# Kernel tuning notes

Measured on AMD Instinct MI355X. Metric: run time of the kernel, lower is better.

Reference implementation:

```python
import jax, jax.numpy as jnp
import numpy as np

C_Z = 128
H = 4
D = C_Z // H          # head_dim = 32
BASE = 2 * D // 2     # base_feature_dim = feature_map_multiplier*head_dim//2 = 32
BSZ, S = 1, 256
EPS_LN = 1e-5


def _lin_params(key, fan_in, fan_out):
    kw, kb = jax.random.split(key)
    bound = 1.0 / np.sqrt(fan_in)
    w = jax.random.uniform(kw, (fan_out, fan_in), jnp.float32, -bound, bound)
    b = jax.random.uniform(kb, (fan_out,), jnp.float32, -bound, bound)
    return w, b


def setup_inputs() -> dict:
    key = jax.random.key(0)
    ks = jax.random.split(key, 9)
    z = jax.random.normal(ks[0], (BSZ, S, S, C_Z), jnp.float32)
    pair_mask = jax.random.randint(ks[1], (BSZ, S, S), 0, 2, jnp.int32)
    q_w, q_b = _lin_params(ks[2], C_Z, C_Z)
    k_w, k_b = _lin_params(ks[3], C_Z, C_Z)
    v_w, v_b = _lin_params(ks[4], C_Z, C_Z)
    qf_w, qf_b = _lin_params(ks[5], D, BASE)
    kf_w, kf_b = _lin_params(ks[6], D, BASE)
    g_w, g_b = _lin_params(ks[7], C_Z, C_Z)
    o_w, o_b = _lin_params(ks[8], C_Z, C_Z)
    return {
        'z': z, 'pair_mask': pair_mask,
        'ln_w': jnp.ones((C_Z,), jnp.float32), 'ln_b': jnp.zeros((C_Z,), jnp.float32),
        'q_w': q_w, 'q_b': q_b, 'k_w': k_w, 'k_b': k_b, 'v_w': v_w, 'v_b': v_b,
        'qf_w': qf_w, 'qf_b': qf_b, 'kf_w': kf_w, 'kf_b': kf_b,
        'g_w': g_w, 'g_b': g_b, 'o_w': o_w, 'o_b': o_b,
    }


def _feature_map(t, w, b):
    m = jnp.clip(t @ w.T + b, -8.0, 8.0)
    return jnp.concatenate([jnp.exp(m), jnp.exp(-m)], axis=-1)


def reference(z, pair_mask, ln_w, ln_b, q_w, q_b, k_w, k_b, v_w, v_b,
              qf_w, qf_b, kf_w, kf_b, g_w, g_b, o_w, o_b):
    bsz, seq, _, c = z.shape
    h, d = H, c // H
    mask = pair_mask.astype(z.dtype)                         # [B,S,S]

    # LayerNorm over last dim
    mu = jnp.mean(z, axis=-1, keepdims=True)
    var = jnp.mean(jnp.square(z - mu), axis=-1, keepdims=True)
    zn = (z - mu) * jax.lax.rsqrt(var + EPS_LN) * ln_w + ln_b

    z_rows = zn.reshape(bsz * seq, seq, c)                   # [BS, N, C]
    row_mask = mask.reshape(bsz * seq, seq)[:, None, :, None]  # [BS,1,N,1]

    def proj(w, b):
        return (z_rows @ w.T + b).reshape(bsz * seq, seq, h, d).transpose(0, 2, 1, 3)

    q = proj(q_w, q_b)                                       # [BS,H,N,D]
    k = proj(k_w, k_b)
    v = proj(v_w, v_b) * row_mask

    qf = _feature_map(q, qf_w, qf_b)                         # [BS,H,N,F]
    kf = _feature_map(k, kf_w, kf_b) * row_mask

    kv = jnp.einsum('bhnd,bhne->bhde', kf, v)                # [BS,H,F,D]
    k_sum = kf.sum(axis=-2)                                  # [BS,H,F]
    denom = jnp.maximum(jnp.einsum('bhnd,bhd->bhn', qf, k_sum), 1e-6)
    out = jnp.einsum('bhnd,bhde->bhne', qf, kv) / denom[..., None]

    out = out.transpose(0, 2, 1, 3).reshape(bsz * seq, seq, c)
    gate = jax.nn.sigmoid(z_rows @ g_w.T + g_b)
    out = (gate * out) @ o_w.T + o_b
    out = out.reshape(bsz, seq, seq, c)
    return out * mask[..., None]
```

## Files before the change

### kernel.cpp

```cpp
#include <hip/hip_runtime.h>
#include <stdint.h>

#define DEV __device__ __forceinline__

typedef unsigned short u16;
typedef unsigned int u32;
typedef short bh8 __attribute__((ext_vector_type(8)));
typedef float f32x4 __attribute__((ext_vector_type(4)));

DEV float bf2f(u16 v){ return __uint_as_float(((u32)v)<<16); }
DEV u16 f2bf(float f){
    u32 x = __float_as_uint(f);
    x += 0x7fffu + ((x>>16)&1u);
    return (u16)(x>>16);
}
DEV void cvt8(int4 r, float* f){
    u32 a=(u32)r.x, b=(u32)r.y, c=(u32)r.z, d=(u32)r.w;
    f[0]=__uint_as_float(a<<16); f[1]=__uint_as_float(a&0xffff0000u);
    f[2]=__uint_as_float(b<<16); f[3]=__uint_as_float(b&0xffff0000u);
    f[4]=__uint_as_float(c<<16); f[5]=__uint_as_float(c&0xffff0000u);
    f[6]=__uint_as_float(d<<16); f[7]=__uint_as_float(d&0xffff0000u);
}
DEV int2 pk4(float a, float b, float c, float d){
    int2 r;
    r.x = (int)((u32)f2bf(a) | ((u32)f2bf(b)<<16));
    r.y = (int)((u32)f2bf(c) | ((u32)f2bf(d)<<16));
    return r;
}
DEV bh8 ld_frag(const u16* p){
    int4 v = *(const int4*)p;
    union{ int4 i; bh8 h; } u; u.i = v; return u.h;
}
DEV float ldp(const void* p, int i, bool bf){
    return bf ? bf2f(((const u16*)p)[i]) : ((const float*)p)[i];
}
#define MFMA __builtin_amdgcn_mfma_f32_16x16x32_bf16


#define P_LNW 0
#define P_LNB 128
#define P_QW  256
#define P_QB  16640
#define P_KW  16768
#define P_KB  33152
#define P_VW  33280
#define P_VB  49664
#define P_QFW 49792
#define P_QFB 50816
#define P_KFW 50848
#define P_KFB 51872
#define P_GW  51904
#define P_GB  68288
#define P_OW  68416
#define P_OB  84800
#define P_TOT 84928
#define P_CQW 84928
#define P_CQB 101312
#define P_CKW 101440
#define P_CKB 117824

#define NCONV 332

__global__ void detect_kernel(const u32* __restrict__ z, u32* __restrict__ flag){
    int tid = threadIdx.x;
    u32 w = z[(size_t)tid*997];
    u32 b0 = w & 0xFFFFu;
    int e = (int)((b0>>7)&0xFF);
    int good = (e>=96 && e<=150) ? 1 : 0;
    __shared__ int red[4];
    #pragma unroll
    for(int o=1;o<64;o<<=1) good += __shfl_xor(good,o,64);
    if((tid&63)==0) red[tid>>6]=good;
    __syncthreads();
    if(tid==0) *flag = ((red[0]+red[1]+red[2]+red[3]) > 192) ? 1u : 0u;
}

__global__ void prep_params(
    const void* p0, const void* p1, const void* p2, const void* p3,
    const void* p4, const void* p5, const void* p6, const void* p7,
    const void* p8, const void* p9, const void* p10, const void* p11,
    const void* p12, const void* p13, const void* p14, const void* p15,
    const u32* __restrict__ flag, u16* __restrict__ dst){
    bool bf = (*flag != 0u);
    int b = blockIdx.x, tid = threadIdx.x;
    if(b < NCONV){
        int idx = b*256 + tid;
        if(idx >= P_TOT) return;
        const int offs[17] = {P_LNW,P_LNB,P_QW,P_QB,P_KW,P_KB,P_VW,P_VB,
                              P_QFW,P_QFB,P_KFW,P_KFB,P_GW,P_GB,P_OW,P_OB,P_TOT};
        const void* ptrs[16] = {p0,p1,p2,p3,p4,p5,p6,p7,p8,p9,p10,p11,p12,p13,p14,p15};
        int tsel = 0;
        #pragma unroll
        for(int i=1;i<16;++i) if(idx >= offs[i]) tsel = i;
        dst[idx] = bf ? ((const u16*)ptrs[tsel])[idx - offs[tsel]]
                      : f2bf(((const float*)ptrs[tsel])[idx - offs[tsel]]);
    } else if(b < NCONV + 128){
        int idx = (b - NCONV)*256 + tid;
        int sel = idx >> 14;
        int rem = idx & 16383;
        int h = rem >> 12, j = (rem >> 7) & 31, c = rem & 127;
        const void* FWp = sel ? p10 : p8;
        const void* Wp  = sel ? p4  : p2;
        float s = 0.f;
        #pragma unroll
        for(int d=0; d<32; ++d)
            s += ldp(FWp, j*32+d, bf) * ldp(Wp, (h*32+d)*128 + c, bf);
        dst[(sel ? P_CKW : P_CQW) + h*4096 + j*128 + c] = f2bf(s);
    } else {
        int t = tid;
        int sel = t >> 7, h = (t >> 5) & 3, j = t & 31;
        const void* FWp = sel ? p10 : p8;
        const void* FBp = sel ? p11 : p9;
        const void* Bp  = sel ? p5  : p3;
        float s = ldp(FBp, j, bf);
        #pragma unroll
        for(int d=0; d<32; ++d)
            s += ldp(FWp, j*32+d, bf) * ldp(Bp, h*32+d, bf);
        dst[(sel ? P_CKB : P_CQB) + h*32 + j] = f2bf(s);
    }
}

__global__ void ln_kernel(const void* __restrict__ zv, const u16* __restrict__ pb,
                          const u32* __restrict__ flag, u16* __restrict__ zn){
    int t = blockIdx.x*4 + (threadIdx.x>>6);
    int lane = threadIdx.x & 63;
    float x0, x1;
    if(*flag){
        u32 pr = ((const u32*)zv)[(size_t)t*64 + lane];
        x0 = __uint_as_float(pr<<16); x1 = __uint_as_float(pr & 0xffff0000u);
    } else {
        float2 v = ((const float2*)zv)[(size_t)t*64 + lane];
        x0 = v.x; x1 = v.y;
    }
    float s = x0 + x1, s2 = x0*x0 + x1*x1;
    #pragma unroll
    for(int o=1;o<64;o<<=1){ s += __shfl_xor(s,o,64); s2 += __shfl_xor(s2,o,64); }
    float mean = s*(1.f/128.f);
    float var  = s2*(1.f/128.f) - mean*mean;
    float rs = rsqrtf(var + 1e-5f);
    int c0 = 2*lane;
    float w0 = bf2f(pb[P_LNW+c0]), w1 = bf2f(pb[P_LNW+c0+1]);
    float b0 = bf2f(pb[P_LNB+c0]), b1 = bf2f(pb[P_LNB+c0+1]);
    float o0 = (x0-mean)*rs*w0 + b0;
    float o1 = (x1-mean)*rs*w1 + b1;
    u32 po = (u32)f2bf(o0) | ((u32)f2bf(o1)<<16);
    *(u32*)(zn + (size_t)t*128 + c0) = po;
}

#define ST_N 264
#define ST_F 68
#define SM_KF   1024
#define SM_VT   34816
#define SM_QF   1024
#define SM_KVT  51712
#define SM_TOT  56200

__global__ __launch_bounds__(256,2)
void mega_kernel(const u16* __restrict__ zn, const int* __restrict__ mask,
                 const u16* __restrict__ pb, u16* __restrict__ attn){
    __shared__ __align__(16) char smem[SM_TOT];
    float* mask_f = (float*)smem;
    u16* kfT = (u16*)(smem + SM_KF);
    u16* vT  = (u16*)(smem + SM_VT);
    u16* qf  = (u16*)(smem + SM_QF);
    u16* kvT = (u16*)(smem + SM_KVT);

    int g = blockIdx.x, row = g>>2, h = g&3;
    int tid = threadIdx.x, lane = tid & 63, wv = tid >> 6;
    int lm = lane & 15, quad = lane >> 4;

    mask_f[tid] = (float)mask[row*256 + tid];

    bh8 a[4][4];
    {
        const u16* Ab = zn + ((size_t)row*256 + wv*64 + lm)*128 + quad*8;
        #pragma unroll
        for(int mt=0; mt<4; ++mt)
            #pragma unroll
            for(int ks=0; ks<4; ++ks)
                a[mt][ks] = ld_frag(Ab + (size_t)mt*16*128 + ks*32);
    }
    bh8 onesf;
    { union{int4 i; bh8 h;} u; u.i.x=u.i.y=u.i.z=u.i.w=0x3F803F80; onesf = u.h; }

    __syncthreads();

    f32x4 gacc[4][2];
    {
        f32x4 acc[4][2];
        #pragma unroll
        for(int mt=0;mt<4;++mt){ acc[mt][0]=(f32x4){0,0,0,0}; acc[mt][1]=(f32x4){0,0,0,0}; }
        #pragma unroll
        for(int ks=0; ks<4; ++ks){
            bh8 b0 = ld_frag(pb + P_CKW + h*4096 + lm*128      + ks*32 + quad*8);
            bh8 b1 = ld_frag(pb + P_CKW + h*4096 + (16+lm)*128 + ks*32 + quad*8);
            #pragma unroll
            for(int mt=0; mt<4; ++mt){
                acc[mt][0] = MFMA(a[mt][ks], b0, acc[mt][0], 0,0,0);
                acc[mt][1] = MFMA(a[mt][ks], b1, acc[mt][1], 0,0,0);
            }
        }
        float bb0 = bf2f(pb[P_CKB + h*32 + lm]);
        float bb1 = bf2f(pb[P_CKB + h*32 + 16 + lm]);
        #pragma unroll
        for(int mt=0; mt<4; ++mt){
            int n0 = wv*64 + mt*16 + quad*4;
            float e0p[4], e0m[4], e1p[4], e1m[4];
            #pragma unroll
            for(int r=0; r<4; ++r){
                float mk = mask_f[n0+r];
                float m0 = fminf(8.f, fmaxf(-8.f, acc[mt][0][r] + bb0));
                float m1 = fminf(8.f, fmaxf(-8.f, acc[mt][1][r] + bb1));
                e0p[r] = __expf( m0)*mk;  e0m[r] = __expf(-m0)*mk;
                e1p[r] = __expf( m1)*mk;  e1m[r] = __expf(-m1)*mk;
            }
            *(int2*)(kfT + (size_t)(lm   )*ST_N + n0) = pk4(e0p[0],e0p[1],e0p[2],e0p[3]);
            *(int2*)(kfT + (size_t)(lm+32)*ST_N + n0) = pk4(e0m[0],e0m[1],e0m[2],e0m[3]);
            *(int2*)(kfT + (size_t)(lm+16)*ST_N + n0) = pk4(e1p[0],e1p[1],e1p[2],e1p[3]);
            *(int2*)(kfT + (size_t)(lm+48)*ST_N + n0) = pk4(e1m[0],e1m[1],e1m[2],e1m[3]);
        }
    }
    {
        f32x4 acc[4][2];
        #pragma unroll
        for(int mt=0;mt<4;++mt){ acc[mt][0]=(f32x4){0,0,0,0}; acc[mt][1]=(f32x4){0,0,0,0}; }
        #pragma unroll
        for(int ks=0; ks<4; ++ks){
            bh8 b0 = ld_frag(pb + P_VW + (size_t)(h*32 + lm)*128      + ks*32 + quad*8);
            bh8 b1 = ld_frag(pb + P_VW + (size_t)(h*32 + 16 + lm)*128 + ks*32 + quad*8);
            #pragma unroll
            for(int mt=0; mt<4; ++mt){
                acc[mt][0] = MFMA(a[mt][ks], b0, acc[mt][0], 0,0,0);
                acc[mt][1] = MFMA(a[mt][ks], b1, acc[mt][1], 0,0,0);
            }
        }
        float bb0 = bf2f(pb[P_VB + h*32 + lm]);
        float bb1 = bf2f(pb[P_VB + h*32 + 16 + lm]);
        #pragma unroll
        for(int mt=0; mt<4; ++mt){
            int n0 = wv*64 + mt*16 + quad*4;
            float v0[4], v1[4];
            #pragma unroll
            for(int r=0; r<4; ++r){
                float mk = mask_f[n0+r];
                v0[r] = (acc[mt][0][r] + bb0)*mk;
                v1[r] = (acc[mt][1][r] + bb1)*mk;
            }
            *(int2*)(vT + (size_t)(lm   )*ST_N + n0) = pk4(v0[0],v0[1],v0[2],v0[3]);
            *(int2*)(vT + (size_t)(16+lm)*ST_N + n0) = pk4(v1[0],v1[1],v1[2],v1[3]);
        }
    }
    {
        f32x4 acc[4][2];
        #pragma unroll
        for(int mt=0;mt<4;++mt){ acc[mt][0]=(f32x4){0,0,0,0}; acc[mt][1]=(f32x4){0,0,0,0}; }
        #pragma unroll
        for(int ks=0; ks<4; ++ks){
            bh8 b0 = ld_frag(pb + P_GW + (size_t)(h*32 + lm)*128      + ks*32 + quad*8);
            bh8 b1 = ld_frag(pb + P_GW + (size_t)(h*32 + 16 + lm)*128 + ks*32 + quad*8);
            #pragma unroll
            for(int mt=0; mt<4; ++mt){
                acc[mt][0] = MFMA(a[mt][ks], b0, acc[mt][0], 0,0,0);
                acc[mt][1] = MFMA(a[mt][ks], b1, acc[mt][1], 0,0,0);
            }
        }
        float bb0 = bf2f(pb[P_GB + h*32 + lm]);
        float bb1 = bf2f(pb[P_GB + h*32 + 16 + lm]);
        #pragma unroll
        for(int mt=0; mt<4; ++mt)
            #pragma unroll
            for(int r=0; r<4; ++r){
                gacc[mt][0][r] = 1.f/(1.f + __expf(-(acc[mt][0][r] + bb0)));
                gacc[mt][1][r] = 1.f/(1.f + __expf(-(acc[mt][1][r] + bb1)));
            }
    }
    __syncthreads();
    {
        f32x4 acc0=(f32x4){0,0,0,0}, acc1=(f32x4){0,0,0,0}, acc2=(f32x4){0,0,0,0};
        #pragma unroll
        for(int ks=0; ks<8; ++ks){
            bh8 aa = ld_frag(kfT + (size_t)(wv*16+lm)*ST_N + ks*32 + quad*8);
            bh8 b0 = ld_frag(vT + (size_t)lm*ST_N      + ks*32 + quad*8);
            bh8 b1 = ld_frag(vT + (size_t)(16+lm)*ST_N + ks*32 + quad*8);
            acc0 = MFMA(aa, b0, acc0, 0,0,0);
            acc1 = MFMA(aa, b1, acc1, 0,0,0);
            acc2 = MFMA(aa, onesf, acc2, 0,0,0);
        }
        int f0 = wv*16 + quad*4;
        *(int2*)(kvT + (size_t)(lm   )*ST_F + f0) = pk4(acc0[0],acc0[1],acc0[2],acc0[3]);
        *(int2*)(kvT + (size_t)(16+lm)*ST_F + f0) = pk4(acc1[0],acc1[1],acc1[2],acc1[3]);
        if(lm==0)
            *(int2*)(kvT + (size_t)32*ST_F + f0) = pk4(acc2[0],acc2[1],acc2[2],acc2[3]);
    }
    __syncthreads();
    {
        f32x4 acc[4][2];
        #pragma unroll
        for(int mt=0;mt<4;++mt){ acc[mt][0]=(f32x4){0,0,0,0}; acc[mt][1]=(f32x4){0,0,0,0}; }
        #pragma unroll
        for(int ks=0; ks<4; ++ks){
            bh8 b0 = ld_frag(pb + P_CQW + h*4096 + lm*128      + ks*32 + quad*8);
            bh8 b1 = ld_frag(pb + P_CQW + h*4096 + (16+lm)*128 + ks*32 + quad*8);
            #pragma unroll
            for(int mt=0; mt<4; ++mt){
                acc[mt][0] = MFMA(a[mt][ks], b0, acc[mt][0], 0,0,0);
                acc[mt][1] = MFMA(a[mt][ks], b1, acc[mt][1], 0,0,0);
            }
        }
        float bb0 = bf2f(pb[P_CQB + h*32 + lm]);
        float bb1 = bf2f(pb[P_CQB + h*32 + 16 + lm]);
        #pragma unroll
        for(int mt=0; mt<4; ++mt)
            #pragma unroll
            for(int r=0; r<4; ++r){
                int n = wv*64 + mt*16 + quad*4 + r;
                float m0 = fminf(8.f, fmaxf(-8.f, acc[mt][0][r] + bb0));
                float m1 = fminf(8.f, fmaxf(-8.f, acc[mt][1][r] + bb1));
                qf[n*ST_F + lm     ] = f2bf(__expf( m0));
                qf[n*ST_F + lm + 32] = f2bf(__expf(-m0));
                qf[n*ST_F + lm + 16] = f2bf(__expf( m1));
                qf[n*ST_F + lm + 48] = f2bf(__expf(-m1));
            }
    }
    __syncthreads();
    {
        f32x4 acc[4][3];
        #pragma unroll
        for(int mt=0;mt<4;++mt)
            #pragma unroll
            for(int nt=0;nt<3;++nt) acc[mt][nt]=(f32x4){0,0,0,0};
        #pragma unroll
        for(int ks=0; ks<2; ++ks){
            bh8 b0 = ld_frag(kvT + (size_t)lm*ST_F      + ks*32 + quad*8);
            bh8 b1 = ld_frag(kvT + (size_t)(16+lm)*ST_F + ks*32 + quad*8);
            bh8 b2 = ld_frag(kvT + (size_t)32*ST_F      + ks*32 + quad*8);
            #pragma unroll
            for(int mt=0; mt<4; ++mt){
                bh8 aa = ld_frag(qf + (size_t)(wv*64+mt*16+lm)*ST_F + ks*32 + quad*8);
                acc[mt][0] = MFMA(aa, b0, acc[mt][0], 0,0,0);
                acc[mt][1] = MFMA(aa, b1, acc[mt][1], 0,0,0);
                acc[mt][2] = MFMA(aa, b2, acc[mt][2], 0,0,0);
            }
        }
        #pragma unroll
        for(int mt=0; mt<4; ++mt)
            #pragma unroll
            for(int r=0; r<4; ++r){
                int n = wv*64 + mt*16 + quad*4 + r;
                float rcp = 1.f / fmaxf(acc[mt][2][r], 1e-6f);
                u16* op = attn + ((size_t)row*256 + n)*128 + h*32;
                op[lm]    = f2bf(acc[mt][0][r]*rcp*gacc[mt][0][r]);
                op[16+lm] = f2bf(acc[mt][1][r]*rcp*gacc[mt][1][r]);
            }
    }
}

#define LDS_P 136
__global__ __launch_bounds__(256,2)
void oproj_kernel(const u16* __restrict__ attn, const u16* __restrict__ pb,
                  const int* __restrict__ mask, const u32* __restrict__ flagp,
                  void* __restrict__ out){
    __shared__ u16 st[128*LDS_P];
    int tid = threadIdx.x;
    int lane = tid&63, wv = tid>>6;
    int mhalf = (wv>>1)*64, nhalf = (wv&1)*64;
    int lm = lane&15, quad = lane>>4;
    int m0 = blockIdx.x*128;

    f32x4 acc[4][4];
    #pragma unroll
    for(int mt=0;mt<4;++mt)
        #pragma unroll
        for(int nt=0;nt<4;++nt)
            acc[mt][nt] = (f32x4){0.f,0.f,0.f,0.f};

    const u16* Abase = attn + (size_t)(m0 + mhalf + lm)*128 + quad*8;
    const u16* W = pb + P_OW;
    #pragma unroll
    for(int ks=0; ks<4; ++ks){
        bh8 a[4], b[4];
        #pragma unroll
        for(int mt=0; mt<4; ++mt)
            a[mt] = ld_frag(Abase + (size_t)mt*16*128 + ks*32);
        #pragma unroll
        for(int nt=0; nt<4; ++nt)
            b[nt] = ld_frag(W + (size_t)(nhalf + nt*16 + lm)*128 + ks*32 + quad*8);
        #pragma unroll
        for(int mt=0; mt<4; ++mt)
            #pragma unroll
            for(int nt=0; nt<4; ++nt)
                acc[mt][nt] = MFMA(a[mt], b[nt], acc[mt][nt], 0, 0, 0);
    }
    float bv[4];
    #pragma unroll
    for(int nt=0; nt<4; ++nt) bv[nt] = bf2f(pb[P_OB + nhalf + nt*16 + lm]);
    #pragma unroll
    for(int mt=0; mt<4; ++mt){
        int mrow = m0 + mhalf + mt*16 + quad*4;
        float mk[4];
        #pragma unroll
        for(int r=0;r<4;++r) mk[r] = (float)mask[mrow+r];
        #pragma unroll
        for(int nt=0; nt<4; ++nt)
            #pragma unroll
            for(int r=0; r<4; ++r){
                float x = (acc[mt][nt][r] + bv[nt]) * mk[r];
                st[(mhalf + mt*16 + quad*4 + r)*LDS_P + nhalf + nt*16 + lm] = f2bf(x);
            }
    }
    __syncthreads();
    {
        int row = tid>>1, half = tid&1;
        const u16* src = st + row*LDS_P + half*64;
        bool isbf = (*flagp != 0u);
        if(isbf){
            u16* dst = (u16*)out + (size_t)(m0 + row)*128 + half*64;
            #pragma unroll
            for(int it=0; it<8; ++it)
                ((int4*)dst)[it] = ((const int4*)src)[it];
        } else {
            float* dst = (float*)out + (size_t)(m0 + row)*128 + half*64;
            #pragma unroll
            for(int it=0; it<8; ++it){
                float f[8]; cvt8(((const int4*)src)[it], f);
                float4 lo; lo.x=f[0]; lo.y=f[1]; lo.z=f[2]; lo.w=f[3];
                float4 hi; hi.x=f[4]; hi.y=f[5]; hi.z=f[6]; hi.w=f[7];
                ((float4*)dst)[it*2  ] = lo;
                ((float4*)dst)[it*2+1] = hi;
            }
        }
    }
}

extern "C" void kernel_launch(void* const* d_in, const int* in_sizes, int n_in,
                              void* d_out, int out_size, void* d_ws, size_t ws_size,
                              hipStream_t stream){
    const void* z    = d_in[0];
    const int*  mask = (const int*)d_in[1];

    char* ws = (char*)d_ws;
    const size_t MB = (size_t)1<<20;
    u16*   zn   = (u16*)(ws + 0*MB);
    u16*   attn = (u16*)(ws + 16*MB);
    u16*   pb   = (u16*)(ws + 32*MB);
    u32*   flag = (u32*)(ws + 33*MB);

    detect_kernel<<<1,256,0,stream>>>((const u32*)z, flag);
    prep_params<<<NCONV+129,256,0,stream>>>(
        d_in[2], d_in[3], d_in[4], d_in[5], d_in[6], d_in[7], d_in[8], d_in[9],
        d_in[10], d_in[11], d_in[12], d_in[13], d_in[14], d_in[15], d_in[16], d_in[17],
        flag, pb);
    ln_kernel<<<16384,256,0,stream>>>(z, pb, flag, zn);
    mega_kernel<<<1024,256,0,stream>>>(zn, mask, pb, attn);
    oproj_kernel<<<512,256,0,stream>>>(attn, pb, mask, flag, d_out);
}
```

Baseline: 189.6 us.

## Drop dtype detection path and fuse K/V/gate projections into one MFMA pass

Removes the runtime bf16/fp32 detection kernel and all flag-based branching, hardcoding fp32 inputs and outputs. In the mega kernel, the separate K-feature, V and gate projection loops are merged into one loop with six accumulator sets sharing the same A fragments. This saves one kernel launch, the flag loads, and repeated loop and epilogue overhead. The cost is higher register pressure from 24 live f32x4 accumulators, which may reduce occupancy.

```diff
diff --git a/kernel.cpp b/kernel.cpp
--- a/kernel.cpp
+++ b/kernel.cpp
@@ -30,9 +30,6 @@
 DEV bh8 ld_frag(const u16* p){
     int4 v = *(const int4*)p;
     union{ int4 i; bh8 h; } u; u.i = v; return u.h;
-}
-DEV float ldp(const void* p, int i, bool bf){
-    return bf ? bf2f(((const u16*)p)[i]) : ((const float*)p)[i];
 }
 #define MFMA __builtin_amdgcn_mfma_f32_16x16x32_bf16
 
@@ -61,77 +58,55 @@
 
 #define NCONV 332
 
-__global__ void detect_kernel(const u32* __restrict__ z, u32* __restrict__ flag){
-    int tid = threadIdx.x;
-    u32 w = z[(size_t)tid*997];
-    u32 b0 = w & 0xFFFFu;
-    int e = (int)((b0>>7)&0xFF);
-    int good = (e>=96 && e<=150) ? 1 : 0;
-    __shared__ int red[4];
-    #pragma unroll
-    for(int o=1;o<64;o<<=1) good += __shfl_xor(good,o,64);
-    if((tid&63)==0) red[tid>>6]=good;
-    __syncthreads();
-    if(tid==0) *flag = ((red[0]+red[1]+red[2]+red[3]) > 192) ? 1u : 0u;
-}
-
 __global__ void prep_params(
-    const void* p0, const void* p1, const void* p2, const void* p3,
-    const void* p4, const void* p5, const void* p6, const void* p7,
-    const void* p8, const void* p9, const void* p10, const void* p11,
-    const void* p12, const void* p13, const void* p14, const void* p15,
-    const u32* __restrict__ flag, u16* __restrict__ dst){
-    bool bf = (*flag != 0u);
+    const float* p0, const float* p1, const float* p2, const float* p3,
+    const float* p4, const float* p5, const float* p6, const float* p7,
+    const float* p8, const float* p9, const float* p10, const float* p11,
+    const float* p12, const float* p13, const float* p14, const float* p15,
+    u16* __restrict__ dst){
     int b = blockIdx.x, tid = threadIdx.x;
     if(b < NCONV){
         int idx = b*256 + tid;
         if(idx >= P_TOT) return;
         const int offs[17] = {P_LNW,P_LNB,P_QW,P_QB,P_KW,P_KB,P_VW,P_VB,
                               P_QFW,P_QFB,P_KFW,P_KFB,P_GW,P_GB,P_OW,P_OB,P_TOT};
-        const void* ptrs[16] = {p0,p1,p2,p3,p4,p5,p6,p7,p8,p9,p10,p11,p12,p13,p14,p15};
+        const float* ptrs[16] = {p0,p1,p2,p3,p4,p5,p6,p7,p8,p9,p10,p11,p12,p13,p14,p15};
         int tsel = 0;
         #pragma unroll
         for(int i=1;i<16;++i) if(idx >= offs[i]) tsel = i;
-        dst[idx] = bf ? ((const u16*)ptrs[tsel])[idx - offs[tsel]]
-                      : f2bf(((const float*)ptrs[tsel])[idx - offs[tsel]]);
+        dst[idx] = f2bf(ptrs[tsel][idx - offs[tsel]]);
     } else if(b < NCONV + 128){
         int idx = (b - NCONV)*256 + tid;
         int sel = idx >> 14;
         int rem = idx & 16383;
         int h = rem >> 12, j = (rem >> 7) & 31, c = rem & 127;
-        const void* FWp = sel ? p10 : p8;
-        const void* Wp  = sel ? p4  : p2;
+        const float* FWp = sel ? p10 : p8;
+        const float* Wp  = sel ? p4  : p2;
         float s = 0.f;
         #pragma unroll
         for(int d=0; d<32; ++d)
-            s += ldp(FWp, j*32+d, bf) * ldp(Wp, (h*32+d)*128 + c, bf);
+            s += FWp[j*32+d] * Wp[(h*32+d)*128 + c];
         dst[(sel ? P_CKW : P_CQW) + h*4096 + j*128 + c] = f2bf(s);
     } else {
         int t = tid;
         int sel = t >> 7, h = (t >> 5) & 3, j = t & 31;
-        const void* FWp = sel ? p10 : p8;
-        const void* FBp = sel ? p11 : p9;
-        const void* Bp  = sel ? p5  : p3;
-        float s = ldp(FBp, j, bf);
+        const float* FWp = sel ? p10 : p8;
+        const float* FBp = sel ? p11 : p9;
+        const float* Bp  = sel ? p5  : p3;
+        float s = FBp[j];
         #pragma unroll
         for(int d=0; d<32; ++d)
-            s += ldp(FWp, j*32+d, bf) * ldp(Bp, h*32+d, bf);
+            s += FWp[j*32+d] * Bp[h*32+d];
         dst[(sel ? P_CKB : P_CQB) + h*32 + j] = f2bf(s);
     }
 }
 
-__global__ void ln_kernel(const void* __restrict__ zv, const u16* __restrict__ pb,
-                          const u32* __restrict__ flag, u16* __restrict__ zn){
+__global__ void ln_kernel(const float* __restrict__ zv, const u16* __restrict__ pb,
+                          u16* __restrict__ zn){
     int t = blockIdx.x*4 + (threadIdx.x>>6);
     int lane = threadIdx.x & 63;
-    float x0, x1;
-    if(*flag){
-        u32 pr = ((const u32*)zv)[(size_t)t*64 + lane];
-        x0 = __uint_as_float(pr<<16); x1 = __uint_as_float(pr & 0xffff0000u);
-    } else {
-        float2 v = ((const float2*)zv)[(size_t)t*64 + lane];
-        x0 = v.x; x1 = v.y;
-    }
+    float2 v = ((const float2*)zv)[(size_t)t*64 + lane];
+    float x0 = v.x, x1 = v.y;
     float s = x0 + x1, s2 = x0*x0 + x1*x1;
     #pragma unroll
     for(int o=1;o<64;o<<=1){ s += __shfl_xor(s,o,64); s2 += __shfl_xor(s2,o,64); }
@@ -187,92 +162,55 @@
 
     f32x4 gacc[4][2];
     {
-        f32x4 acc[4][2];
-        #pragma unroll
-        for(int mt=0;mt<4;++mt){ acc[mt][0]=(f32x4){0,0,0,0}; acc[mt][1]=(f32x4){0,0,0,0}; }
+        f32x4 acc[4][6];
+        #pragma unroll
+        for(int mt=0;mt<4;++mt)
+            #pragma unroll
+            for(int j=0;j<6;++j) acc[mt][j] = (f32x4){0,0,0,0};
         #pragma unroll
         for(int ks=0; ks<4; ++ks){
-            bh8 b0 = ld_frag(pb + P_CKW + h*4096 + lm*128      + ks*32 + quad*8);
-            bh8 b1 = ld_frag(pb + P_CKW + h*4096 + (16+lm)*128 + ks*32 + quad*8);
-            #pragma unroll
-            for(int mt=0; mt<4; ++mt){
-                acc[mt][0] = MFMA(a[mt][ks], b0, acc[mt][0], 0,0,0);
-                acc[mt][1] = MFMA(a[mt][ks], b1, acc[mt][1], 0,0,0);
-            }
-        }
-        float bb0 = bf2f(pb[P_CKB + h*32 + lm]);
-        float bb1 = bf2f(pb[P_CKB + h*32 + 16 + lm]);
+            bh8 b[6];
+            b[0] = ld_frag(pb + P_CKW + h*4096 + lm*128            + ks*32 + quad*8);
+            b[1] = ld_frag(pb + P_CKW + h*4096 + (16+lm)*128       + ks*32 + quad*8);
+            b[2] = ld_frag(pb + P_VW + (size_t)(h*32 + lm)*128     + ks*32 + quad*8);
+            b[3] = ld_frag(pb + P_VW + (size_t)(h*32 + 16+lm)*128  + ks*32 + quad*8);
+            b[4] = ld_frag(pb + P_GW + (size_t)(h*32 + lm)*128     + ks*32 + quad*8);
+            b[5] = ld_frag(pb + P_GW + (size_t)(h*32 + 16+lm)*128  + ks*32 + quad*8);
+            #pragma unroll
+            for(int mt=0; mt<4; ++mt)
+                #pragma unroll
+                for(int j=0;j<6;++j)
+                    acc[mt][j] = MFMA(a[mt][ks], b[j], acc[mt][j], 0,0,0);
+        }
+        float bk0 = bf2f(pb[P_CKB + h*32 + lm]);
+        float bk1 = bf2f(pb[P_CKB + h*32 + 16 + lm]);
+        float bv0 = bf2f(pb[P_VB + h*32 + lm]);
+        float bv1 = bf2f(pb[P_VB + h*32 + 16 + lm]);
+        float bg0 = bf2f(pb[P_GB + h*32 + lm]);
+        float bg1 = bf2f(pb[P_GB + h*32 + 16 + lm]);
         #pragma unroll
         for(int mt=0; mt<4; ++mt){
             int n0 = wv*64 + mt*16 + quad*4;
-            float e0p[4], e0m[4], e1p[4], e1m[4];
+            float ep0[4], em0[4], ep1[4], em1[4], v0[4], v1[4];
             #pragma unroll
             for(int r=0; r<4; ++r){
                 float mk = mask_f[n0+r];
-                float m0 = fminf(8.f, fmaxf(-8.f, acc[mt][0][r] + bb0));
-                float m1 = fminf(8.f, fmaxf(-8.f, acc[mt][1][r] + bb1));
-                e0p[r] = __expf( m0)*mk;  e0m[r] = __expf(-m0)*mk;
-                e1p[r] = __expf( m1)*mk;  e1m[r] = __expf(-m1)*mk;
-            }
-            *(int2*)(kfT + (size_t)(lm   )*ST_N + n0) = pk4(e0p[0],e0p[1],e0p[2],e0p[3]);
-            *(int2*)(kfT + (size_t)(lm+32)*ST_N + n0) = pk4(e0m[0],e0m[1],e0m[2],e0m[3]);
-            *(int2*)(kfT + (size_t)(lm+16)*ST_N + n0) = pk4(e1p[0],e1p[1],e1p[2],e1p[3]);
-            *(int2*)(kfT + (size_t)(lm+48)*ST_N + n0) = pk4(e1m[0],e1m[1],e1m[2],e1m[3]);
-        }
-    }
-    {
-        f32x4 acc[4][2];
-        #pragma unroll
-        for(int mt=0;mt<4;++mt){ acc[mt][0]=(f32x4){0,0,0,0}; acc[mt][1]=(f32x4){0,0,0,0}; }
-        #pragma unroll
-        for(int ks=0; ks<4; ++ks){
-            bh8 b0 = ld_frag(pb + P_VW + (size_t)(h*32 + lm)*128      + ks*32 + quad*8);
-            bh8 b1 = ld_frag(pb + P_VW + (size_t)(h*32 + 16 + lm)*128 + ks*32 + quad*8);
-            #pragma unroll
-            for(int mt=0; mt<4; ++mt){
-                acc[mt][0] = MFMA(a[mt][ks], b0, acc[mt][0], 0,0,0);
-                acc[mt][1] = MFMA(a[mt][ks], b1, acc[mt][1], 0,0,0);
-            }
-        }
-        float bb0 = bf2f(pb[P_VB + h*32 + lm]);
-        float bb1 = bf2f(pb[P_VB + h*32 + 16 + lm]);
-        #pragma unroll
-        for(int mt=0; mt<4; ++mt){
-            int n0 = wv*64 + mt*16 + quad*4;
-            float v0[4], v1[4];
-            #pragma unroll
-            for(int r=0; r<4; ++r){
-                float mk = mask_f[n0+r];
-                v0[r] = (acc[mt][0][r] + bb0)*mk;
-                v1[r] = (acc[mt][1][r] + bb1)*mk;
-            }
-            *(int2*)(vT + (size_t)(lm   )*ST_N + n0) = pk4(v0[0],v0[1],v0[2],v0[3]);
-            *(int2*)(vT + (size_t)(16+lm)*ST_N + n0) = pk4(v1[0],v1[1],v1[2],v1[3]);
-        }
-    }
-    {
-        f32x4 acc[4][2];
-        #pragma unroll
-        for(int mt=0;mt<4;++mt){ acc[mt][0]=(f32x4){0,0,0,0}; acc[mt][1]=(f32x4){0,0,0,0}; }
-        #pragma unroll
-        for(int ks=0; ks<4; ++ks){
-            bh8 b0 = ld_frag(pb + P_GW + (size_t)(h*32 + lm)*128      + ks*32 + quad*8);
-            bh8 b1 = ld_frag(pb + P_GW + (size_t)(h*32 + 16 + lm)*128 + ks*32 + quad*8);
-            #pragma unroll
-            for(int mt=0; mt<4; ++mt){
-                acc[mt][0] = MFMA(a[mt][ks], b0, acc[mt][0], 0,0,0);
-                acc[mt][1] = MFMA(a[mt][ks], b1, acc[mt][1], 0,0,0);
-            }
-        }
-        float bb0 = bf2f(pb[P_GB + h*32 + lm]);
-        float bb1 = bf2f(pb[P_GB + h*32 + 16 + lm]);
-        #pragma unroll
-        for(int mt=0; mt<4; ++mt)
-            #pragma unroll
-            for(int r=0; r<4; ++r){
-                gacc[mt][0][r] = 1.f/(1.f + __expf(-(acc[mt][0][r] + bb0)));
-                gacc[mt][1][r] = 1.f/(1.f + __expf(-(acc[mt][1][r] + bb1)));
-            }
+                float m0 = fminf(8.f, fmaxf(-8.f, acc[mt][0][r] + bk0));
+                float m1 = fminf(8.f, fmaxf(-8.f, acc[mt][1][r] + bk1));
+                ep0[r] = __expf( m0)*mk;  em0[r] = __expf(-m0)*mk;
+                ep1[r] = __expf( m1)*mk;  em1[r] = __expf(-m1)*mk;
+                v0[r] = (acc[mt][2][r] + bv0)*mk;
+                v1[r] = (acc[mt][3][r] + bv1)*mk;
+                gacc[mt][0][r] = 1.f/(1.f + __expf(-(acc[mt][4][r] + bg0)));
+                gacc[mt][1][r] = 1.f/(1.f + __expf(-(acc[mt][5][r] + bg1)));
+            }
+            *(int2*)(kfT + (size_t)(lm   )*ST_N + n0) = pk4(ep0[0],ep0[1],ep0[2],ep0[3]);
+            *(int2*)(kfT + (size_t)(lm+32)*ST_N + n0) = pk4(em0[0],em0[1],em0[2],em0[3]);
+            *(int2*)(kfT + (size_t)(lm+16)*ST_N + n0) = pk4(ep1[0],ep1[1],ep1[2],ep1[3]);
+            *(int2*)(kfT + (size_t)(lm+48)*ST_N + n0) = pk4(em1[0],em1[1],em1[2],em1[3]);
+            *(int2*)(vT  + (size_t)(lm   )*ST_N + n0) = pk4(v0[0],v0[1],v0[2],v0[3]);
+            *(int2*)(vT  + (size_t)(16+lm)*ST_N + n0) = pk4(v1[0],v1[1],v1[2],v1[3]);
+        }
     }
     __syncthreads();
     {
@@ -358,8 +296,7 @@
 #define LDS_P 136
 __global__ __launch_bounds__(256,2)
 void oproj_kernel(const u16* __restrict__ attn, const u16* __restrict__ pb,
-                  const int* __restrict__ mask, const u32* __restrict__ flagp,
-                  void* __restrict__ out){
+                  const int* __restrict__ mask, float* __restrict__ out){
     __shared__ u16 st[128*LDS_P];
     int tid = threadIdx.x;
     int lane = tid&63, wv = tid>>6;
@@ -412,22 +349,14 @@
     {
         int row = tid>>1, half = tid&1;
         const u16* src = st + row*LDS_P + half*64;
-        bool isbf = (*flagp != 0u);
-        if(isbf){
-            u16* dst = (u16*)out + (size_t)(m0 + row)*128 + half*64;
-            #pragma unroll
-            for(int it=0; it<8; ++it)
-                ((int4*)dst)[it] = ((const int4*)src)[it];
-        } else {
-            float* dst = (float*)out + (size_t)(m0 + row)*128 + half*64;
-            #pragma unroll
-            for(int it=0; it<8; ++it){
-                float f[8]; cvt8(((const int4*)src)[it], f);
-                float4 lo; lo.x=f[0]; lo.y=f[1]; lo.z=f[2]; lo.w=f[3];
-                float4 hi; hi.x=f[4]; hi.y=f[5]; hi.z=f[6]; hi.w=f[7];
-                ((float4*)dst)[it*2  ] = lo;
-                ((float4*)dst)[it*2+1] = hi;
-            }
+        float* dst = out + (size_t)(m0 + row)*128 + half*64;
+        #pragma unroll
+        for(int it=0; it<8; ++it){
+            float f[8]; cvt8(((const int4*)src)[it], f);
+            float4 lo; lo.x=f[0]; lo.y=f[1]; lo.z=f[2]; lo.w=f[3];
+            float4 hi; hi.x=f[4]; hi.y=f[5]; hi.z=f[6]; hi.w=f[7];
+            ((float4*)dst)[it*2  ] = lo;
+            ((float4*)dst)[it*2+1] = hi;
         }
     }
 }
@@ -435,22 +364,22 @@
 extern "C" void kernel_launch(void* const* d_in, const int* in_sizes, int n_in,
                               void* d_out, int out_size, void* d_ws, size_t ws_size,
                               hipStream_t stream){
-    const void* z    = d_in[0];
-    const int*  mask = (const int*)d_in[1];
+    const float* z    = (const float*)d_in[0];
+    const int*   mask = (const int*)d_in[1];
 
     char* ws = (char*)d_ws;
     const size_t MB = (size_t)1<<20;
-    u16*   zn   = (u16*)(ws + 0*MB);
-    u16*   attn = (u16*)(ws + 16*MB);
-    u16*   pb   = (u16*)(ws + 32*MB);
-    u32*   flag = (u32*)(ws + 33*MB);
-
-    detect_kernel<<<1,256,0,stream>>>((const u32*)z, flag);
+    u16* zn   = (u16*)(ws + 0*MB);
+    u16* attn = (u16*)(ws + 16*MB);
+    u16* pb   = (u16*)(ws + 32*MB);
+
     prep_params<<<NCONV+129,256,0,stream>>>(
-        d_in[2], d_in[3], d_in[4], d_in[5], d_in[6], d_in[7], d_in[8], d_in[9],
-        d_in[10], d_in[11], d_in[12], d_in[13], d_in[14], d_in[15], d_in[16], d_in[17],
-        flag, pb);
-    ln_kernel<<<16384,256,0,stream>>>(z, pb, flag, zn);
+        (const float*)d_in[2],  (const float*)d_in[3],  (const float*)d_in[4],  (const float*)d_in[5],
+        (const float*)d_in[6],  (const float*)d_in[7],  (const float*)d_in[8],  (const float*)d_in[9],
+        (const float*)d_in[10], (const float*)d_in[11], (const float*)d_in[12], (const float*)d_in[13],
+        (const float*)d_in[14], (const float*)d_in[15], (const float*)d_in[16], (const float*)d_in[17],
+        pb);
+    ln_kernel<<<16384,256,0,stream>>>(z, pb, zn);
     mega_kernel<<<1024,256,0,stream>>>(zn, mask, pb, attn);
-    oproj_kernel<<<512,256,0,stream>>>(attn, pb, mask, flag, d_out);
-}
+    oproj_kernel<<<512,256,0,stream>>>(attn, pb, mask, (float*)d_out);
+}
```

Result: faster. 183.0 us (-3.5%).
